# Kernel optimization log

Measured on AMD Instinct MI355X. Metric: run time of the kernel, lower is better.

## Reference

```python
import jax, jax.numpy as jnp
import numpy as np

NUM_HEADS = 16
HEAD_DIM = 128  # 2048 // 16


def setup_inputs() -> dict:
    key = jax.random.key(0)
    ks = jax.random.split(key, 5)
    B, S, D = 2, 2048, 2048
    scale = 0.02
    return {
        "inputs": jax.random.normal(ks[0], (B, S, D), dtype=jnp.float32),
        "attention_mask": jnp.ones((B, S), dtype=jnp.float32),
        "Wq": jax.random.normal(ks[1], (D, D), dtype=jnp.float32) * scale,
        "Wk": jax.random.normal(ks[2], (D, D), dtype=jnp.float32) * scale,
        "Wv": jax.random.normal(ks[3], (D, D), dtype=jnp.float32) * scale,
        "Wo": jax.random.normal(ks[4], (D, D), dtype=jnp.float32) * scale,
    }


def reference(inputs, attention_mask, Wq, Wk, Wv, Wo):
    B, S, D = inputs.shape
    H, Dh = NUM_HEADS, HEAD_DIM

    def proj(W):
        # nn.Linear: x @ W.T -> [B,S,H,Dh] -> [B,H,S,Dh]
        return (inputs @ W.T).reshape(B, S, H, Dh).transpose(0, 2, 1, 3)

    q, k, v = proj(Wq), proj(Wk), proj(Wv)

    scores = jnp.einsum("bhqd,bhkd->bhqk", q, k) * (1.0 / jnp.sqrt(jnp.float32(Dh)))

    # ALiBi bias: slopes[h] * (pos_q - pos_k), subtracted from scores
    slopes = 2.0 ** (-8.0 * jnp.arange(1, H + 1, dtype=jnp.float32) / H)
    pos = jnp.arange(S, dtype=jnp.float32)
    pos_diff = pos[:, None] - pos[None, :]              # [S,S]
    scores = scores - slopes[None, :, None, None] * pos_diff[None, None, :, :]

    # causal mask: add -inf above the diagonal
    causal = jnp.where(jnp.triu(jnp.ones((S, S), dtype=bool), k=1), -jnp.inf, 0.0)
    scores = scores + causal[None, None, :, :]

    # original multiplies scores by the mask (broadcast over key axis)
    scores = scores * attention_mask[:, None, None, :]

    weights = jax.nn.softmax(scores, axis=-1)
    attn = jnp.einsum("bhqk,bhkd->bhqd", weights, v)
    attn = attn.transpose(0, 2, 1, 3).reshape(B, S, D)
    return attn @ Wo.T
```

## Files before the change

kernel.cpp:

```cpp
#include <hip/hip_runtime.h>
#include <hip/hip_bf16.h>
#include <stdint.h>

using bf16 = __bf16;
using bf16x8 = __attribute__((ext_vector_type(8))) __bf16;
using bf16x4 = __attribute__((ext_vector_type(4))) __bf16;
using f32x4  = __attribute__((ext_vector_type(4))) float;
using u16x8  = __attribute__((ext_vector_type(8))) unsigned short;

#define MFMA16(a,b,c) __builtin_amdgcn_mfma_f32_16x16x32_bf16((a),(b),(c),0,0,0)

__device__ __forceinline__ void gll16(const void* g, void* l) {
  __builtin_amdgcn_global_load_lds(
      (const __attribute__((address_space(1))) uint32_t*)g,
      (__attribute__((address_space(3))) uint32_t*)l, 16, 0, 0);
}

__global__ __launch_bounds__(256) void f32_to_bf16_k(
    const float* __restrict__ in, bf16* __restrict__ out, int n4) {
  int i = blockIdx.x * blockDim.x + threadIdx.x;
  if (i >= n4) return;
  const float4 v = ((const float4*)in)[i];
  bf16x4 o;
  o[0] = (bf16)v.x; o[1] = (bf16)v.y; o[2] = (bf16)v.z; o[3] = (bf16)v.w;
  ((bf16x4*)out)[i] = o;
}

template <typename OutT>
__global__ __launch_bounds__(256, 2) void gemm_bt(
    const bf16* __restrict__ A,
    const bf16* __restrict__ B0, const bf16* __restrict__ B1, const bf16* __restrict__ B2,
    OutT* __restrict__ C0, OutT* __restrict__ C1, OutT* __restrict__ C2,
    int M, int N, int K) {
  const bf16* Bm = (blockIdx.z == 0) ? B0 : (blockIdx.z == 1 ? B1 : B2);
  OutT* C = (blockIdx.z == 0) ? C0 : (blockIdx.z == 1 ? C1 : C2);

  __shared__ bf16 As[128 * 32];
  __shared__ bf16 Bs[128 * 32];

  const int t = threadIdx.x;
  const int w = t >> 6;
  const int l = t & 63;
  const int m0 = blockIdx.y * 128;
  const int n0 = blockIdx.x * 128;
  const int wr = (w >> 1) * 64;
  const int wc = (w & 1) * 64;

  f32x4 acc[4][4] = {};

  const int srow = w * 32 + (l >> 2);
  const int scol = (l & 3) * 8;
  const bf16* Ag = A + (int64_t)(m0 + srow) * K + scol;
  const bf16* Bg = Bm + (int64_t)(n0 + srow) * K + scol;

  const int ar = (l & 15) * 32 + (l >> 4) * 8;

  for (int k0 = 0; k0 < K; k0 += 32) {
    gll16(Ag + k0,          As + (w * 2 + 0) * 512);
    gll16(Ag + k0 + 16 * K, As + (w * 2 + 1) * 512);
    gll16(Bg + k0,          Bs + (w * 2 + 0) * 512);
    gll16(Bg + k0 + 16 * K, Bs + (w * 2 + 1) * 512);
    __syncthreads();

    bf16x8 af[4], bfr[4];
#pragma unroll
    for (int mi = 0; mi < 4; ++mi) af[mi] = *(const bf16x8*)&As[(wr + mi * 16) * 32 + ar];
#pragma unroll
    for (int ni = 0; ni < 4; ++ni) bfr[ni] = *(const bf16x8*)&Bs[(wc + ni * 16) * 32 + ar];
#pragma unroll
    for (int mi = 0; mi < 4; ++mi)
#pragma unroll
      for (int ni = 0; ni < 4; ++ni)
        acc[mi][ni] = MFMA16(af[mi], bfr[ni], acc[mi][ni]);
    __syncthreads();
  }

#pragma unroll
  for (int mi = 0; mi < 4; ++mi) {
    const int row = m0 + wr + mi * 16 + (l >> 4) * 4;
#pragma unroll
    for (int ni = 0; ni < 4; ++ni) {
      const int col = n0 + wc + ni * 16 + (l & 15);
#pragma unroll
      for (int j = 0; j < 4; ++j)
        C[(int64_t)(row + j) * N + col] = (OutT)acc[mi][ni][j];
    }
  }
}

__global__ __launch_bounds__(256, 2) void attn_fwd(
    const bf16* __restrict__ Q, const bf16* __restrict__ Kb,
    const bf16* __restrict__ V, const float* __restrict__ mask,
    bf16* __restrict__ O) {
  constexpr int S = 2048, D = 2048, Dh = 128;
  __shared__ bf16 Ks[2][64 * 128];
  __shared__ bf16 Vt[2][128 * 64];
  __shared__ bf16 Pl[4][16 * 68];

  const int t = threadIdx.x, w = t >> 6, l = t & 63;
  const int lq = l & 15, lk = l >> 4;
  const int qt = 31 - blockIdx.x;
  const int q0 = qt * 64;
  const int bh = blockIdx.y, b = bh >> 4, h = bh & 15;
  const int swz = (lq & 7) << 4;

  const int kvp = t & 31;
  const int d80 = (t >> 5) * 8;
  const int d81 = d80 + 64;

  bf16x8 qf[4];
  {
    const bf16* Qrow = Q + (int64_t)(b * S + q0 + w * 16 + lq) * D + h * Dh;
#pragma unroll
    for (int kk = 0; kk < 4; ++kk) qf[kk] = *(const bf16x8*)&Qrow[kk * 32 + lk * 8];
  }

  float mrow[4], lrow[4];
  f32x4 oacc[8] = {};
#pragma unroll
  for (int j = 0; j < 4; ++j) { mrow[j] = -1e30f; lrow[j] = 0.f; }

  const float scale = 0.08838834764831845f;
  const float slope = exp2f(-0.5f * (float)(h + 1));
  const int ntiles = qt + 1;

  bf16x8 vA0, vA1, vB0, vB1;

#define LOAD_V(kt)                                                          \
  {                                                                         \
    const bf16* vb = V + (int64_t)(b * S + (kt) * 64 + 2 * kvp) * D + h * Dh; \
    vA0 = *(const bf16x8*)(vb + d80);                                       \
    vA1 = *(const bf16x8*)(vb + D + d80);                                   \
    vB0 = *(const bf16x8*)(vb + d81);                                       \
    vB1 = *(const bf16x8*)(vb + D + d81);                                   \
  }

#define STAGE_K(kt, buf)                                                    \
  {                                                                         \
    _Pragma("unroll")                                                       \
    for (int i = 0; i < 4; ++i) {                                           \
      const int chunk = 4 * w + i;                                          \
      const int r = chunk * 4 + (l >> 4);                                   \
      const int cbl = ((l & 15) * 16) ^ ((r & 7) << 4);                     \
      gll16(Kb + (int64_t)(b * S + (kt) * 64 + r) * D + h * Dh + (cbl >> 1),\
            &Ks[buf][chunk * 512]);                                         \
    }                                                                       \
  }

#define WRITE_V(buf)                                                        \
  {                                                                         \
    const u16x8 u00 = __builtin_bit_cast(u16x8, vA0);                       \
    const u16x8 u01 = __builtin_bit_cast(u16x8, vA1);                       \
    const u16x8 u10 = __builtin_bit_cast(u16x8, vB0);                       \
    const u16x8 u11 = __builtin_bit_cast(u16x8, vB1);                       \
    char* vtb = (char*)&Vt[buf][0];                                         \
    _Pragma("unroll")                                                       \
    for (int jj = 0; jj < 8; ++jj) {                                        \
      const int co = (4 * kvp) ^ (jj << 4);                                 \
      *(uint32_t*)(vtb + (d80 + jj) * 128 + co) =                           \
          (uint32_t)u00[jj] | ((uint32_t)u01[jj] << 16);                    \
      *(uint32_t*)(vtb + (d81 + jj) * 128 + co) =                           \
          (uint32_t)u10[jj] | ((uint32_t)u11[jj] << 16);                    \
    }                                                                       \
  }

  LOAD_V(0);
  STAGE_K(0, 0);
  WRITE_V(0);
  __syncthreads();

  for (int kt = 0; kt < ntiles; ++kt) {
    const int cb = kt & 1, nb = cb ^ 1;
    const int kv0 = kt * 64;
    const bool pft = (kt + 1 < ntiles);
    if (pft) {
      STAGE_K(kt + 1, nb);
      LOAD_V(kt + 1);
    }

    f32x4 sc[4];
#pragma unroll
    for (int ni = 0; ni < 4; ++ni) {
      const char* krow = (const char*)&Ks[cb][(ni * 16 + lq) * 128];
      f32x4 a = {};
#pragma unroll
      for (int kk = 0; kk < 4; ++kk) {
        bf16x8 kf = *(const bf16x8*)(krow + ((kk * 64 + lk * 16) ^ swz));
        a = MFMA16(qf[kk], kf, a);
      }
      sc[ni] = a;
    }

#pragma unroll
    for (int ni = 0; ni < 4; ++ni) {
      const int kcol = kv0 + ni * 16 + lq;
      const float mval = mask[b * S + kcol];
#pragma unroll
      for (int j = 0; j < 4; ++j) {
        const int qrow = q0 + w * 16 + lk * 4 + j;
        float s = sc[ni][j] * scale - slope * (float)(qrow - kcol);
        s = (kcol > qrow) ? -1e30f : s;
        sc[ni][j] = s * mval;
      }
    }

#pragma unroll
    for (int j = 0; j < 4; ++j) {
      float mj = fmaxf(fmaxf(sc[0][j], sc[1][j]), fmaxf(sc[2][j], sc[3][j]));
#pragma unroll
      for (int d = 1; d < 16; d <<= 1) mj = fmaxf(mj, __shfl_xor(mj, d));
      const float mnew = fmaxf(mrow[j], mj);
      const float r = __expf(mrow[j] - mnew);
      mrow[j] = mnew;
      float ps = 0.f;
#pragma unroll
      for (int ni = 0; ni < 4; ++ni) {
        const float p = __expf(sc[ni][j] - mnew);
        sc[ni][j] = p;
        ps += p;
      }
#pragma unroll
      for (int d = 1; d < 16; d <<= 1) ps += __shfl_xor(ps, d);
      lrow[j] = lrow[j] * r + ps;
#pragma unroll
      for (int df = 0; df < 8; ++df) oacc[df][j] *= r;
    }

#pragma unroll
    for (int ni = 0; ni < 4; ++ni)
#pragma unroll
      for (int j = 0; j < 4; ++j)
        Pl[w][(lk * 4 + j) * 68 + ni * 16 + lq] = (bf16)sc[ni][j];

    bf16x8 pf[2];
#pragma unroll
    for (int k2 = 0; k2 < 2; ++k2)
      pf[k2] = *(const bf16x8*)&Pl[w][lq * 68 + k2 * 32 + lk * 8];

#pragma unroll
    for (int df = 0; df < 8; ++df) {
      const char* vrow = (const char*)&Vt[cb][(df * 16 + lq) * 64];
#pragma unroll
      for (int k2 = 0; k2 < 2; ++k2) {
        bf16x8 vf = *(const bf16x8*)(vrow + ((k2 * 64 + lk * 16) ^ swz));
        oacc[df] = MFMA16(pf[k2], vf, oacc[df]);
      }
    }

    if (pft) WRITE_V(nb);
    __syncthreads();
  }

#pragma unroll
  for (int df = 0; df < 8; ++df) {
#pragma unroll
    for (int j = 0; j < 4; ++j) {
      const float o = oacc[df][j] / lrow[j];
      O[(int64_t)(b * S + q0 + w * 16 + lk * 4 + j) * D + h * Dh + df * 16 + lq] = (bf16)o;
    }
  }
#undef LOAD_V
#undef STAGE_K
#undef WRITE_V
}

extern "C" void kernel_launch(void* const* d_in, const int* in_sizes, int n_in,
                              void* d_out, int out_size, void* d_ws, size_t ws_size,
                              hipStream_t stream) {
  const float* X    = (const float*)d_in[0];
  const float* mask = (const float*)d_in[1];
  const float* Wq   = (const float*)d_in[2];
  const float* Wk   = (const float*)d_in[3];
  const float* Wv   = (const float*)d_in[4];
  const float* Wo   = (const float*)d_in[5];
  float* out = (float*)d_out;

  bf16* ws = (bf16*)d_ws;
  bf16* Xb  = ws;
  bf16* Wqb = ws + 8388608;
  bf16* Wkb = ws + 12582912;
  bf16* Wvb = ws + 16777216;
  bf16* Wob = ws + 20971520;
  bf16* Qb  = ws + 25165824;
  bf16* Kb  = ws + 33554432;
  bf16* Vb  = ws + 41943040;
  bf16* Ab  = ws + 50331648;

  f32_to_bf16_k<<<8192, 256, 0, stream>>>(X,  Xb,  2097152);
  f32_to_bf16_k<<<4096, 256, 0, stream>>>(Wq, Wqb, 1048576);
  f32_to_bf16_k<<<4096, 256, 0, stream>>>(Wk, Wkb, 1048576);
  f32_to_bf16_k<<<4096, 256, 0, stream>>>(Wv, Wvb, 1048576);
  f32_to_bf16_k<<<4096, 256, 0, stream>>>(Wo, Wob, 1048576);

  gemm_bt<bf16><<<dim3(16, 32, 3), 256, 0, stream>>>(
      Xb, Wqb, Wkb, Wvb, Qb, Kb, Vb, 4096, 2048, 2048);

  attn_fwd<<<dim3(32, 32), 256, 0, stream>>>(Qb, Kb, Vb, mask, Ab);

  gemm_bt<float><<<dim3(16, 32, 1), 256, 0, stream>>>(
      Ab, Wob, Wob, Wob, out, out, out, 4096, 2048, 2048);
}
```

Measured before the change: 520.0 us.

## Transpose attention MFMA operands so each lane owns a query row, and remap workgroups

Swaps the MFMA A/B operands in both attention matmuls so each lane holds one query row's scores across key columns. Row-max and row-sum then need only two cross-lane shuffles instead of sixteen, the mask becomes one float4 load, and P and O are written as packed bf16x4 vectors. Both the GEMM and attention kernels also remap block IDs with an XCD-aware permutation (stride by eight) so neighbouring tiles land on the same die and share L2. This adds index arithmetic and assumes the grid size divides by eight.

```diff
diff --git a/kernel.cpp b/kernel.cpp
--- a/kernel.cpp
+++ b/kernel.cpp
@@ -32,8 +32,16 @@
     const bf16* __restrict__ B0, const bf16* __restrict__ B1, const bf16* __restrict__ B2,
     OutT* __restrict__ C0, OutT* __restrict__ C1, OutT* __restrict__ C2,
     int M, int N, int K) {
-  const bf16* Bm = (blockIdx.z == 0) ? B0 : (blockIdx.z == 1 ? B1 : B2);
-  OutT* C = (blockIdx.z == 0) ? C0 : (blockIdx.z == 1 ? C1 : C2);
+  const int gx = gridDim.x, gy = gridDim.y;
+  const int nwg = gx * gy * gridDim.z;
+  int lid = blockIdx.x + gx * (blockIdx.y + gy * blockIdx.z);
+  lid = (lid & 7) * (nwg >> 3) + (lid >> 3);
+  const int bz = lid / (gx * gy);
+  const int rem = lid - bz * (gx * gy);
+  const int by = rem / gx, bx = rem - by * gx;
+
+  const bf16* Bm = (bz == 0) ? B0 : (bz == 1 ? B1 : B2);
+  OutT* C = (bz == 0) ? C0 : (bz == 1 ? C1 : C2);
 
   __shared__ bf16 As[128 * 32];
   __shared__ bf16 Bs[128 * 32];
@@ -41,8 +49,8 @@
   const int t = threadIdx.x;
   const int w = t >> 6;
   const int l = t & 63;
-  const int m0 = blockIdx.y * 128;
-  const int n0 = blockIdx.x * 128;
+  const int m0 = by * 128;
+  const int n0 = bx * 128;
   const int wr = (w >> 1) * 64;
   const int wc = (w & 1) * 64;
 
@@ -99,9 +107,15 @@
 
   const int t = threadIdx.x, w = t >> 6, l = t & 63;
   const int lq = l & 15, lk = l >> 4;
-  const int qt = 31 - blockIdx.x;
+
+  const int nwg = gridDim.x * gridDim.y;
+  int lid = blockIdx.x + gridDim.x * blockIdx.y;
+  lid = (lid & 7) * (nwg >> 3) + (lid >> 3);
+  const int bx = lid & 31, by = lid >> 5;
+
+  const int qt = 31 - bx;
   const int q0 = qt * 64;
-  const int bh = blockIdx.y, b = bh >> 4, h = bh & 15;
+  const int b = by >> 4, h = by & 15;
   const int swz = (lq & 7) << 4;
 
   const int kvp = t & 31;
@@ -115,14 +129,13 @@
     for (int kk = 0; kk < 4; ++kk) qf[kk] = *(const bf16x8*)&Qrow[kk * 32 + lk * 8];
   }
 
-  float mrow[4], lrow[4];
+  float mr = -1e30f, lr = 0.f;
   f32x4 oacc[8] = {};
-#pragma unroll
-  for (int j = 0; j < 4; ++j) { mrow[j] = -1e30f; lrow[j] = 0.f; }
 
   const float scale = 0.08838834764831845f;
   const float slope = exp2f(-0.5f * (float)(h + 1));
   const int ntiles = qt + 1;
+  const int qrow = q0 + w * 16 + lq;
 
   bf16x8 vA0, vA1, vB0, vB1;
 
@@ -186,78 +199,83 @@
 #pragma unroll
       for (int kk = 0; kk < 4; ++kk) {
         bf16x8 kf = *(const bf16x8*)(krow + ((kk * 64 + lk * 16) ^ swz));
-        a = MFMA16(qf[kk], kf, a);
+        a = MFMA16(kf, qf[kk], a);
       }
       sc[ni] = a;
     }
 
 #pragma unroll
     for (int ni = 0; ni < 4; ++ni) {
-      const int kcol = kv0 + ni * 16 + lq;
-      const float mval = mask[b * S + kcol];
+      const float4 mv = *(const float4*)&mask[b * S + kv0 + ni * 16 + lk * 4];
+      const float* mvp = (const float*)&mv;
 #pragma unroll
       for (int j = 0; j < 4; ++j) {
-        const int qrow = q0 + w * 16 + lk * 4 + j;
+        const int kcol = kv0 + ni * 16 + lk * 4 + j;
         float s = sc[ni][j] * scale - slope * (float)(qrow - kcol);
         s = (kcol > qrow) ? -1e30f : s;
-        sc[ni][j] = s * mval;
+        sc[ni][j] = s * mvp[j];
       }
     }
 
-#pragma unroll
-    for (int j = 0; j < 4; ++j) {
-      float mj = fmaxf(fmaxf(sc[0][j], sc[1][j]), fmaxf(sc[2][j], sc[3][j]));
-#pragma unroll
-      for (int d = 1; d < 16; d <<= 1) mj = fmaxf(mj, __shfl_xor(mj, d));
-      const float mnew = fmaxf(mrow[j], mj);
-      const float r = __expf(mrow[j] - mnew);
-      mrow[j] = mnew;
-      float ps = 0.f;
-#pragma unroll
-      for (int ni = 0; ni < 4; ++ni) {
+    float mj = sc[0][0];
+#pragma unroll
+    for (int ni = 0; ni < 4; ++ni)
+#pragma unroll
+      for (int j = 0; j < 4; ++j) mj = fmaxf(mj, sc[ni][j]);
+    mj = fmaxf(mj, __shfl_xor(mj, 16));
+    mj = fmaxf(mj, __shfl_xor(mj, 32));
+    const float mnew = fmaxf(mr, mj);
+    const float r = __expf(mr - mnew);
+    mr = mnew;
+    float ps = 0.f;
+#pragma unroll
+    for (int ni = 0; ni < 4; ++ni)
+#pragma unroll
+      for (int j = 0; j < 4; ++j) {
         const float p = __expf(sc[ni][j] - mnew);
         sc[ni][j] = p;
         ps += p;
       }
-#pragma unroll
-      for (int d = 1; d < 16; d <<= 1) ps += __shfl_xor(ps, d);
-      lrow[j] = lrow[j] * r + ps;
-#pragma unroll
-      for (int df = 0; df < 8; ++df) oacc[df][j] *= r;
-    }
-
-#pragma unroll
-    for (int ni = 0; ni < 4; ++ni)
-#pragma unroll
-      for (int j = 0; j < 4; ++j)
-        Pl[w][(lk * 4 + j) * 68 + ni * 16 + lq] = (bf16)sc[ni][j];
-
-    bf16x8 pf[2];
-#pragma unroll
-    for (int k2 = 0; k2 < 2; ++k2)
-      pf[k2] = *(const bf16x8*)&Pl[w][lq * 68 + k2 * 32 + lk * 8];
+    ps += __shfl_xor(ps, 16);
+    ps += __shfl_xor(ps, 32);
+    lr = lr * r + ps;
+#pragma unroll
+    for (int df = 0; df < 8; ++df)
+#pragma unroll
+      for (int j = 0; j < 4; ++j) oacc[df][j] *= r;
+
+#pragma unroll
+    for (int ni = 0; ni < 4; ++ni) {
+      bf16x4 pb;
+#pragma unroll
+      for (int j = 0; j < 4; ++j) pb[j] = (bf16)sc[ni][j];
+      *(bf16x4*)&Pl[w][lq * 68 + ni * 16 + lk * 4] = pb;
+    }
+
+    bf16x8 pf0 = *(const bf16x8*)&Pl[w][lq * 68 + lk * 8];
+    bf16x8 pf1 = *(const bf16x8*)&Pl[w][lq * 68 + 32 + lk * 8];
 
 #pragma unroll
     for (int df = 0; df < 8; ++df) {
       const char* vrow = (const char*)&Vt[cb][(df * 16 + lq) * 64];
-#pragma unroll
-      for (int k2 = 0; k2 < 2; ++k2) {
-        bf16x8 vf = *(const bf16x8*)(vrow + ((k2 * 64 + lk * 16) ^ swz));
-        oacc[df] = MFMA16(pf[k2], vf, oacc[df]);
-      }
+      bf16x8 vf0 = *(const bf16x8*)(vrow + ((lk * 16) ^ swz));
+      oacc[df] = MFMA16(vf0, pf0, oacc[df]);
+      bf16x8 vf1 = *(const bf16x8*)(vrow + ((64 + lk * 16) ^ swz));
+      oacc[df] = MFMA16(vf1, pf1, oacc[df]);
     }
 
     if (pft) WRITE_V(nb);
     __syncthreads();
   }
 
+  const float inv = 1.0f / lr;
+  bf16* orow = O + (int64_t)(b * S + qrow) * D + h * Dh;
 #pragma unroll
   for (int df = 0; df < 8; ++df) {
-#pragma unroll
-    for (int j = 0; j < 4; ++j) {
-      const float o = oacc[df][j] / lrow[j];
-      O[(int64_t)(b * S + q0 + w * 16 + lk * 4 + j) * D + h * Dh + df * 16 + lq] = (bf16)o;
-    }
+    bf16x4 ob;
+#pragma unroll
+    for (int j = 0; j < 4; ++j) ob[j] = (bf16)(oacc[df][j] * inv);
+    *(bf16x4*)&orow[df * 16 + lk * 4] = ob;
   }
 #undef LOAD_V
 #undef STAGE_K
```

Result: faster. 435.3 us (-16.3%).
